# Kernel tuning notes

Measured on AMD Instinct MI355X. Metric: run time of the kernel, lower is better.

The kernel has to match this reference:

```python
import jax, jax.numpy as jnp
import numpy as np

COMMITMENT_COST = 0.25
CODE_BOOK_SIZE = 1024
EMBED_DIM = 64


def setup_inputs() -> dict:
    key = jax.random.key(0)
    k1, k2 = jax.random.split(key)
    inputs = jax.random.normal(k1, (32, 64, 32, 32), dtype=jnp.float32)
    # matches torch init: uniform(-1/K, 1/K)
    embedding = jax.random.uniform(
        k2, (CODE_BOOK_SIZE, EMBED_DIM), dtype=jnp.float32,
        minval=-1.0 / CODE_BOOK_SIZE, maxval=1.0 / CODE_BOOK_SIZE)
    return {"inputs": inputs, "embedding": embedding}


def reference(inputs, embedding):
    # inputs: [B, D, H, W] -> [B, H, W, D]
    x = jnp.transpose(inputs, (0, 2, 3, 1))
    B, H, W, D = x.shape
    flat = x.reshape(-1, D)                                   # [N, D]
    # ((x - e)**2).mean(-1), without the [N, K, D] broadcast tensor)
    x2 = jnp.sum(flat * flat, axis=1, keepdims=True)          # [N, 1]
    e2 = jnp.sum(embedding * embedding, axis=1)               # [K]
    distances = (x2 - 2.0 * (flat @ embedding.T) + e2) / D    # [N, K]
    encoding_indices = jnp.argmin(distances, axis=1)          # [N]
    quantized = embedding[encoding_indices].reshape(B, H, W, D)
    e_latent_loss = jnp.mean((jax.lax.stop_gradient(quantized) - x) ** 2)
    q_latent_loss = jnp.mean((quantized - jax.lax.stop_gradient(x)) ** 2)
    loss = q_latent_loss + COMMITMENT_COST * e_latent_loss
    # straight-through estimator (training mode); value identical to quantized
    quantized = x + jax.lax.stop_gradient(quantized - x)
    return (loss,
            jnp.transpose(quantized, (0, 3, 1, 2)),
            encoding_indices.reshape(B, -1))
```

## Files before the change

### kernel.cpp

```cpp
#include <hip/hip_runtime.h>


constexpr int D_   = 64;
constexpr int HW   = 1024;
constexpr int K_   = 1024;
constexpr int PTS  = 128;
constexpr int CK   = 512;
constexpr int DH   = 32;
constexpr int SP   = 132;
constexpr int QE   = 2097152;
constexpr int IDX_OFF = 1 + QE;

__global__ __launch_bounds__(1024, 4) void vq_main_kernel(
    const float* __restrict__ in, const float* __restrict__ emb,
    float* __restrict__ out, float* __restrict__ loss_acc,
    unsigned* __restrict__ cnt) {
  __shared__ float eTs[DH * CK];
  __shared__ float xT[D_ * SP];
  __shared__ float e2s[K_];
  __shared__ float x2s[PTS];
  __shared__ int   idx_sel[PTS];
  __shared__ float redbuf[8];

  const int t    = threadIdx.x;
  const int lane = t & 63;
  const int wv   = t >> 6;
  const int p0   = wv * 8;
  const int blk  = blockIdx.x;
  const int b    = blk >> 3;
  const int hw0  = (blk & 7) * PTS;
  const float* inb = in + b * (D_ * HW) + hw0;

  const int kl = t & 511;
  const int h  = t >> 9;
  const int pos = ((kl >> 2) & 1) * 256 + (kl >> 3) * 4 + (kl & 3);

#pragma unroll
  for (int i = 0; i < 2; ++i) {
    int fi = t + i * 1024;
    int d  = fi >> 5, p4 = fi & 31;
    *(float4*)(&xT[d * SP + p4 * 4]) = *(const float4*)(inb + d * HW + p4 * 4);
  }

  {
    const float4* e4 = (const float4*)(emb + t * 64);
    float s = 0.f;
#pragma unroll
    for (int q = 0; q < 16; ++q) {
      float4 v = e4[q];
      s += v.x * v.x; s += v.y * v.y; s += v.z * v.z; s += v.w * v.w;
    }
    e2s[t] = s;
  }

  {
    const float4* g = (const float4*)(emb + kl * 64 + h * 16);
    float4 pf[4];
#pragma unroll
    for (int r = 0; r < 4; ++r) pf[r] = g[r];
#pragma unroll
    for (int r = 0; r < 4; ++r) {
      int dq = h * 16 + r * 4;
      eTs[(dq + 0) * CK + pos] = pf[r].x;
      eTs[(dq + 1) * CK + pos] = pf[r].y;
      eTs[(dq + 2) * CK + pos] = pf[r].z;
      eTs[(dq + 3) * CK + pos] = pf[r].w;
    }
  }
  __syncthreads();

  if (t < PTS) {
    float s = 0.f;
#pragma unroll 8
    for (int d = 0; d < D_; ++d) { float xv = xT[d * SP + t]; s = fmaf(xv, xv, s); }
    x2s[t] = s;
  }
  __syncthreads();

  float minv[8]; int mini[8];
#pragma unroll
  for (int i = 0; i < 8; ++i) { minv[i] = 3.4e38f; mini[i] = 0; }

#pragma unroll 1
  for (int c = 0; c < 2; ++c) {
    float acc[8][8];
#pragma unroll
    for (int i = 0; i < 8; ++i)
#pragma unroll
      for (int j = 0; j < 8; ++j) acc[i][j] = 0.f;

#pragma unroll 1
    for (int dh = 0; dh < 2; ++dh) {
      const int s = c * 2 + dh;
      float4 pf[4];
      if (s < 3) {
        const int cn = (s + 1) >> 1, dn = (s + 1) & 1;
        const float4* g =
            (const float4*)(emb + (cn * CK + kl) * 64 + dn * DH + h * 16);
#pragma unroll
        for (int r = 0; r < 4; ++r) pf[r] = g[r];
      }

      const float* ep = &eTs[lane * 4];
      const float* xp = &xT[dh * DH * SP + p0];
#pragma unroll 8
      for (int dd = 0; dd < DH; ++dd) {
        float4 e0 = *(const float4*)(ep);
        float4 e1 = *(const float4*)(ep + 256);
        float4 xa = *(const float4*)(xp);
        float4 xb = *(const float4*)(xp + 4);
        ep += CK; xp += SP;
        float xf[8] = {xa.x, xa.y, xa.z, xa.w, xb.x, xb.y, xb.z, xb.w};
        float ef[8] = {e0.x, e0.y, e0.z, e0.w, e1.x, e1.y, e1.z, e1.w};
#pragma unroll
        for (int i = 0; i < 8; ++i)
#pragma unroll
          for (int j = 0; j < 8; ++j)
            acc[i][j] = fmaf(xf[i], ef[j], acc[i][j]);
      }

      if (s < 3) {
        __syncthreads();
#pragma unroll
        for (int r = 0; r < 4; ++r) {
          int dq = h * 16 + r * 4;
          eTs[(dq + 0) * CK + pos] = pf[r].x;
          eTs[(dq + 1) * CK + pos] = pf[r].y;
          eTs[(dq + 2) * CK + pos] = pf[r].z;
          eTs[(dq + 3) * CK + pos] = pf[r].w;
        }
        __syncthreads();
      }
    }

    float x2v[8];
    {
      float4 xa = *(const float4*)&x2s[p0];
      float4 xb = *(const float4*)&x2s[p0 + 4];
      x2v[0]=xa.x; x2v[1]=xa.y; x2v[2]=xa.z; x2v[3]=xa.w;
      x2v[4]=xb.x; x2v[5]=xb.y; x2v[6]=xb.z; x2v[7]=xb.w;
    }
    float e2f[8];
    {
      const float4* p4 = (const float4*)&e2s[c * CK + lane * 8];
      float4 v0 = p4[0], v1 = p4[1];
      e2f[0]=v0.x; e2f[1]=v0.y; e2f[2]=v0.z; e2f[3]=v0.w;
      e2f[4]=v1.x; e2f[5]=v1.y; e2f[6]=v1.z; e2f[7]=v1.w;
    }
#pragma unroll
    for (int j = 0; j < 8; ++j) {
      int cg = c * CK + lane * 8 + j;
      float e2v = e2f[j];
#pragma unroll
      for (int i = 0; i < 8; ++i) {
        float u = fmaf(-2.f, acc[i][j], x2v[i]) + e2v;
        if (u < minv[i]) { minv[i] = u; mini[i] = cg; }
      }
    }
  }

#pragma unroll
  for (int i = 0; i < 8; ++i) {
    float v = minv[i]; int ix = mini[i];
#pragma unroll
    for (int off = 1; off < 64; off <<= 1) {
      float vo = __shfl_xor(v, off);
      int   io = __shfl_xor(ix, off);
      if (vo < v || (vo == v && io < ix)) { v = vo; ix = io; }
    }
    if (lane == 0) idx_sel[p0 + i] = ix;
  }
  __syncthreads();

  if (t < PTS) out[IDX_OFF + blk * PTS + t] = (float)idx_sel[t];

  float* outq = out + 1 + b * (D_ * HW) + hw0;
  float lp = 0.f;
  if (t < 512) {
#pragma unroll
    for (int i = 0; i < 4; ++i) {
      int fi = t + i * 512;
      int p = fi & 127, qd = fi >> 7;
      int cidx = idx_sel[p];
      float4 q = *(const float4*)(emb + cidx * 64 + qd * 4);
      float xv0 = xT[(qd * 4 + 0) * SP + p];
      float xv1 = xT[(qd * 4 + 1) * SP + p];
      float xv2 = xT[(qd * 4 + 2) * SP + p];
      float xv3 = xT[(qd * 4 + 3) * SP + p];
      float d0 = q.x - xv0, d1 = q.y - xv1, d2 = q.z - xv2, d3 = q.w - xv3;
      lp = fmaf(d0, d0, lp); lp = fmaf(d1, d1, lp);
      lp = fmaf(d2, d2, lp); lp = fmaf(d3, d3, lp);
      outq[(qd * 4 + 0) * HW + p] = xv0 + d0;
      outq[(qd * 4 + 1) * HW + p] = xv1 + d1;
      outq[(qd * 4 + 2) * HW + p] = xv2 + d2;
      outq[(qd * 4 + 3) * HW + p] = xv3 + d3;
    }

#pragma unroll
    for (int off = 1; off < 64; off <<= 1) lp += __shfl_xor(lp, off);
    if ((t & 63) == 0) redbuf[t >> 6] = lp;
  }
  __syncthreads();
  if (t == 0) {
    float part = 0.f;
#pragma unroll
    for (int w = 0; w < 8; ++w) part += redbuf[w];
    atomicAdd(loss_acc, part);
    __threadfence();
    unsigned old = atomicAdd(cnt, 1u);
    if (old == 255u) {
      __threadfence();
      float total = atomicAdd(loss_acc, 0.0f);
      float m = total * (1.0f / 2097152.0f);
      out[0] = m + 0.25f * m;
    }
  }
}

extern "C" void kernel_launch(void* const* d_in, const int* in_sizes, int n_in,
                              void* d_out, int out_size, void* d_ws, size_t ws_size,
                              hipStream_t stream) {
  const float* in  = (const float*)d_in[0];
  const float* emb = (const float*)d_in[1];
  float* out = (float*)d_out;
  float* loss_acc = (float*)d_ws;
  unsigned* cnt   = (unsigned*)d_ws + 4;

  hipMemsetAsync(d_ws, 0, 64, stream);
  vq_main_kernel<<<256, 1024, 0, stream>>>(in, emb, out, loss_acc, cnt);
}
```

Before: 154.1 us.

## Drop register prefetch of next codebook chunk and reduce inner unroll

Global loads of the next codebook chunk used to be issued before the FMA loop and held in registers across it. They now happen after the barrier, directly before the shared-memory stores. The inner dot-product loop unroll also drops from 8 to 2. This is meant to cut register pressure for the 1024-thread blocks, at the cost of exposing global load latency at each chunk swap.

Result: faster. 138.1 us (-10.4%).

```diff
diff --git a/kernel.cpp b/kernel.cpp
--- a/kernel.cpp
+++ b/kernel.cpp
@@ -55,17 +55,16 @@
 
   {
     const float4* g = (const float4*)(emb + kl * 64 + h * 16);
-    float4 pf[4];
-#pragma unroll
-    for (int r = 0; r < 4; ++r) pf[r] = g[r];
-#pragma unroll
-    for (int r = 0; r < 4; ++r) {
-      int dq = h * 16 + r * 4;
-      eTs[(dq + 0) * CK + pos] = pf[r].x;
-      eTs[(dq + 1) * CK + pos] = pf[r].y;
-      eTs[(dq + 2) * CK + pos] = pf[r].z;
-      eTs[(dq + 3) * CK + pos] = pf[r].w;
-    }
+    float4 v0 = g[0], v1 = g[1], v2 = g[2], v3 = g[3];
+    int dq = h * 16;
+    eTs[(dq + 0) * CK + pos] = v0.x; eTs[(dq + 1) * CK + pos] = v0.y;
+    eTs[(dq + 2) * CK + pos] = v0.z; eTs[(dq + 3) * CK + pos] = v0.w;
+    eTs[(dq + 4) * CK + pos] = v1.x; eTs[(dq + 5) * CK + pos] = v1.y;
+    eTs[(dq + 6) * CK + pos] = v1.z; eTs[(dq + 7) * CK + pos] = v1.w;
+    eTs[(dq + 8) * CK + pos] = v2.x; eTs[(dq + 9) * CK + pos] = v2.y;
+    eTs[(dq +10) * CK + pos] = v2.z; eTs[(dq +11) * CK + pos] = v2.w;
+    eTs[(dq +12) * CK + pos] = v3.x; eTs[(dq +13) * CK + pos] = v3.y;
+    eTs[(dq +14) * CK + pos] = v3.z; eTs[(dq +15) * CK + pos] = v3.w;
   }
   __syncthreads();
 
@@ -92,18 +91,10 @@
 #pragma unroll 1
     for (int dh = 0; dh < 2; ++dh) {
       const int s = c * 2 + dh;
-      float4 pf[4];
-      if (s < 3) {
-        const int cn = (s + 1) >> 1, dn = (s + 1) & 1;
-        const float4* g =
-            (const float4*)(emb + (cn * CK + kl) * 64 + dn * DH + h * 16);
-#pragma unroll
-        for (int r = 0; r < 4; ++r) pf[r] = g[r];
-      }
 
       const float* ep = &eTs[lane * 4];
       const float* xp = &xT[dh * DH * SP + p0];
-#pragma unroll 8
+#pragma unroll 2
       for (int dd = 0; dd < DH; ++dd) {
         float4 e0 = *(const float4*)(ep);
         float4 e1 = *(const float4*)(ep + 256);
@@ -121,14 +112,19 @@
 
       if (s < 3) {
         __syncthreads();
-#pragma unroll
-        for (int r = 0; r < 4; ++r) {
-          int dq = h * 16 + r * 4;
-          eTs[(dq + 0) * CK + pos] = pf[r].x;
-          eTs[(dq + 1) * CK + pos] = pf[r].y;
-          eTs[(dq + 2) * CK + pos] = pf[r].z;
-          eTs[(dq + 3) * CK + pos] = pf[r].w;
-        }
+        const int cn = (s + 1) >> 1, dn = (s + 1) & 1;
+        const float4* g =
+            (const float4*)(emb + (cn * CK + kl) * 64 + dn * DH + h * 16);
+        float4 v0 = g[0], v1 = g[1], v2 = g[2], v3 = g[3];
+        int dq = h * 16;
+        eTs[(dq + 0) * CK + pos] = v0.x; eTs[(dq + 1) * CK + pos] = v0.y;
+        eTs[(dq + 2) * CK + pos] = v0.z; eTs[(dq + 3) * CK + pos] = v0.w;
+        eTs[(dq + 4) * CK + pos] = v1.x; eTs[(dq + 5) * CK + pos] = v1.y;
+        eTs[(dq + 6) * CK + pos] = v1.z; eTs[(dq + 7) * CK + pos] = v1.w;
+        eTs[(dq + 8) * CK + pos] = v2.x; eTs[(dq + 9) * CK + pos] = v2.y;
+        eTs[(dq +10) * CK + pos] = v2.z; eTs[(dq +11) * CK + pos] = v2.w;
+        eTs[(dq +12) * CK + pos] = v3.x; eTs[(dq +13) * CK + pos] = v3.y;
+        eTs[(dq +14) * CK + pos] = v3.z; eTs[(dq +15) * CK + pos] = v3.w;
         __syncthreads();
       }
     }
```
